# Optimization experiments

Measured on AMD Instinct MI355X. Metric: run time of the kernel, lower is better.

The kernel has to match this reference:

```python
import jax, jax.numpy as jnp
import numpy as np

FP = 2048       # fingerprint / hopf_input_size
A = 1024        # hopf_asso_dim (num_heads = 1)
B = 512         # batch of molecules
T = 50000       # number of templates (memory size)
BETA = 0.125    # hopf_beta


def setup_inputs() -> dict:
    key = jax.random.key(0)
    k_m, k_t, k_wm, k_wt = jax.random.split(key, 4)
    # binary-ish fingerprints approximated with uniform [0,1)
    m = jax.random.uniform(k_m, (B, FP), dtype=jnp.float32)
    templates = jax.random.uniform(k_t, (T, FP), dtype=jnp.float32)
    # kaiming_normal fan_in linear: std = 1/sqrt(fan_in)
    std = 1.0 / np.sqrt(FP)
    W_mol = jax.random.normal(k_wm, (A, FP), dtype=jnp.float32) * std
    b_mol = jnp.zeros((A,), dtype=jnp.float32)
    W_temp = jax.random.normal(k_wt, (A, FP), dtype=jnp.float32) * std
    b_temp = jnp.zeros((A,), dtype=jnp.float32)
    return {"m": m, "templates": templates, "W_mol": W_mol, "b_mol": b_mol,
            "W_temp": W_temp, "b_temp": b_temp}


def reference(m, templates, W_mol, b_mol, W_temp, b_temp):
    # mol encoder: single Linear (last layer -> no activation, dropout=0 eval)
    Xi = m @ W_mol.T + b_mol                 # [B, A] queries
    # template encoder: single Linear -> stored pattern memory
    X = templates @ W_temp.T + b_temp       # [T, A] keys/memory
    # Hopfield association: beta-scaled similarity = logits over templates
    out = BETA * jnp.einsum('ba,ta->bt', Xi, X)   # [B, T]
    return out
```

## Files before the change

kernel.cpp:

```cpp
#include <hip/hip_runtime.h>
#include <cstdint>
#include <cstddef>

typedef __attribute__((ext_vector_type(8))) short short8;
typedef __attribute__((ext_vector_type(8))) _Float16 f16x8;
typedef __attribute__((ext_vector_type(4))) float f32x4;
typedef __attribute__((ext_vector_type(4))) unsigned short u16x4;
typedef unsigned short u16;

#define FP_  2048
#define AD_  1024
#define BB_  512
#define TT_  50000
#define BETA_ 0.125f

__device__ __forceinline__ u16 f2bf(float x){
  uint32_t u = __builtin_bit_cast(uint32_t, x);
  u = (u + 0x7fffu + ((u >> 16) & 1u)) >> 16;
  return (u16)u;
}
__device__ __forceinline__ u16 f2h_bits(float x){
  _Float16 h = (_Float16)x;
  return __builtin_bit_cast(u16, h);
}
__device__ __forceinline__ unsigned int pkrtz_u32(float a, float b){
  return __builtin_bit_cast(unsigned int, __builtin_amdgcn_cvt_pkrtz(a, b));
}

__device__ __forceinline__ void gload_lds16(const void* g, void* l){
  __builtin_amdgcn_global_load_lds((const __attribute__((address_space(1))) void*)g,
                                   (__attribute__((address_space(3))) void*)l,
                                   16, 0, 0);
}

#define SB   __builtin_amdgcn_s_barrier()
#define SCH  __builtin_amdgcn_sched_barrier(0)
#define WAIT_LGKM0 asm volatile("s_waitcnt lgkmcnt(0)" ::: "memory")
#define WAIT_VM(n) asm volatile("s_waitcnt vmcnt(" #n ")" ::: "memory")

__global__ void conv_bf_k(const float* __restrict__ src, u16* __restrict__ dst, int n){
  int i = (blockIdx.x * blockDim.x + threadIdx.x) * 4;
  if (i >= n) return;
  f32x4 v = *reinterpret_cast<const f32x4*>(src + i);
  u16x4 h;
  #pragma unroll
  for (int e = 0; e < 4; ++e) h[e] = f2bf(v[e]);
  *reinterpret_cast<u16x4*>(dst + i) = h;
}

__global__ void conv_bf_T_k(const float* __restrict__ W, u16* __restrict__ outT,
                            int R, int C){
  __shared__ float tile[32][33];
  int c0 = blockIdx.x * 32;
  int r0 = blockIdx.y * 32;
  int tx = threadIdx.x;
  int ty = threadIdx.y;
  #pragma unroll
  for (int i = 0; i < 32; i += 8)
    tile[ty + i][tx] = W[(size_t)(r0 + ty + i) * C + c0 + tx];
  __syncthreads();
  #pragma unroll
  for (int i = 0; i < 32; i += 8){
    float x = tile[tx][ty + i];
    outT[(size_t)(c0 + ty + i) * R + r0 + tx] = f2bf(x);
  }
}

__global__ void dot_rows_k(const float* __restrict__ Xi, const float* __restrict__ bt,
                           float* __restrict__ c, int K){
  int row  = blockIdx.x * 4 + (threadIdx.x >> 6);
  int lane = threadIdx.x & 63;
  float s = 0.f;
  for (int a = lane; a < K; a += 64) s += Xi[(size_t)row * K + a] * bt[a];
  #pragma unroll
  for (int off = 32; off; off >>= 1) s += __shfl_down(s, off);
  if (lane == 0) c[row] = s;
}

template<int TM, int TN, int FM, int FN, int OUT>
__global__ __launch_bounds__(256, 2)
void gemm_s(const u16* __restrict__ A, const u16* __restrict__ B,
            int M, int N, int K,
            float* __restrict__ Cf, u16* __restrict__ C16,
            const float* __restrict__ colBias)
{
  constexpr int BK = 32;
  constexpr int WM = TM / (16 * FM);
  constexpr int WN = TN / (16 * FN);
  static_assert(WM * WN == 4, "4 waves / 256 threads");
  constexpr int BUFE = (TM + TN) * BK;

  __shared__ __align__(16) u16 lds[2 * BUFE];

  const int m0 = blockIdx.x * TM;
  const int n0 = blockIdx.y * TN;

  const int tid  = threadIdx.x;
  const int w    = tid >> 6;
  const int lane = tid & 63;
  const int lr   = lane & 15;
  const int lg   = lane >> 4;
  const int wm   = w / WN;
  const int wn   = w % WN;

  const int rrA = tid >> 2;
  const int chA = tid & 3;

  short8 ra, rb;

  f32x4 acc[FM][FN];
  #pragma unroll
  for (int i = 0; i < FM; ++i)
    #pragma unroll
    for (int j = 0; j < FN; ++j)
      acc[i][j] = (f32x4){0.f, 0.f, 0.f, 0.f};

  auto stage_load = [&](int k0){
    int gm = m0 + rrA;
    ra = *reinterpret_cast<const short8*>(A + (size_t)gm * K + k0 + chA * 8);
    int gn = n0 + rrA; if (gn > N - 1) gn = N - 1;
    rb = *reinterpret_cast<const short8*>(B + (size_t)gn * K + k0 + chA * 8);
  };
  auto stage_store = [&](int buf){
    u16* As = lds + buf * BUFE;
    u16* Bs = As + TM * BK;
    int row = rrA;
    int sw  = (chA ^ ((row >> 1) & 3)) << 3;
    *reinterpret_cast<short8*>(As + row * BK + sw) = ra;
    *reinterpret_cast<short8*>(Bs + row * BK + sw) = rb;
  };

  const int NT = K / BK;
  stage_load(0);
  stage_store(0);
  __syncthreads();

  int cur = 0;
  for (int t = 0; t < NT; ++t){
    const bool have_next = (t + 1 < NT);
    if (have_next) stage_load((t + 1) * BK);

    u16* As = lds + cur * BUFE;
    u16* Bs = As + TM * BK;

    short8 ah[FM], bh[FN];
    #pragma unroll
    for (int i = 0; i < FM; ++i){
      int row = wm * FM * 16 + i * 16 + lr;
      int off = row * BK + ((lg ^ ((row >> 1) & 3)) << 3);
      ah[i] = *reinterpret_cast<short8*>(As + off);
    }
    #pragma unroll
    for (int j = 0; j < FN; ++j){
      int row = wn * FN * 16 + j * 16 + lr;
      int off = row * BK + ((lg ^ ((row >> 1) & 3)) << 3);
      bh[j] = *reinterpret_cast<short8*>(Bs + off);
    }
    #pragma unroll
    for (int i = 0; i < FM; ++i)
      #pragma unroll
      for (int j = 0; j < FN; ++j)
        acc[i][j] = __builtin_amdgcn_mfma_f32_16x16x32_bf16(ah[i], bh[j], acc[i][j], 0, 0, 0);

    if (have_next){
      __builtin_amdgcn_sched_barrier(0);
      stage_store(cur ^ 1);
      __syncthreads();
    }
    cur ^= 1;
  }

  #pragma unroll
  for (int i = 0; i < FM; ++i){
    int rbase = m0 + wm * FM * 16 + i * 16 + lg * 4;
    #pragma unroll
    for (int j = 0; j < FN; ++j){
      int gcol = n0 + wn * FN * 16 + j * 16 + lr;
      if (gcol < N){
        float cb = colBias ? colBias[gcol] : 0.f;
        #pragma unroll
        for (int r = 0; r < 4; ++r){
          int grow = rbase + r;
          float v = acc[i][j][r] + cb;
          size_t idx = (size_t)grow * N + gcol;
          if constexpr (OUT == 1){
            Cf[idx]  = v;
            C16[idx] = f2bf(v);
          } else {
            C16[idx] = f2h_bits(v);
          }
        }
      }
    }
  }
}

__global__ __launch_bounds__(512, 1)
void gemm_big(const u16* __restrict__ Ah,
              const float* __restrict__ Bf,
              float* __restrict__ C,
              const float* __restrict__ rowAdd, float alpha)
{
  constexpr int K = FP_, NN = TT_;
  constexpr int NT = K / 64;
  constexpr int KS = 8192;
  constexpr int BOFF = 16384;
  constexpr int SLOT = 32768;

  __shared__ __align__(16) u16 lds[2 * SLOT];

  int id  = blockIdx.x;
  int xcd = id & 7;
  int g   = id >> 3;
  int mt  = g & 1;
  int sg  = g >> 1;
  int strips = (xcd < 4) ? 25 : 24;
  if (sg >= strips) return;
  int nt = ((xcd < 4) ? xcd * 25 : 100 + (xcd - 4) * 24) + sg;
  const int m0 = mt * 256;
  const int n0 = nt * 256;

  const int tid  = threadIdx.x;
  const int w    = tid >> 6;
  const int lane = tid & 63;
  const int lr   = lane & 15;
  const int lg   = lane >> 4;
  const int wm   = w >> 2;
  const int wn   = w & 3;

  auto glA = [&](u16* sp_, int Tt, int h){
    int rl = lane >> 2;
    int cc = lane & 3;
    int row = h * 128 + w * 16 + rl;
    #pragma unroll
    for (int ks = 0; ks < 2; ++ks){
      const u16* src = Ah + (size_t)(m0 + row) * K + Tt * 64 + ks * 32
                     + ((cc ^ ((row >> 1) & 3)) << 3);
      gload_lds16(src, sp_ + ks * KS + (size_t)(h * 128 + w * 16) * 32);
    }
  };
  auto issueB = [&](int Tt, int h, f32x4 (&rb)[4]){
    #pragma unroll
    for (int p = 0; p < 4; ++p){
      int rl = h * 128 + p * 32 + (tid >> 4);
      int gn = n0 + rl; if (gn > NN - 1) gn = NN - 1;
      rb[p] = *reinterpret_cast<const f32x4*>(Bf + (size_t)gn * K + Tt * 64 + (tid & 15) * 4);
    }
  };
  auto publishB = [&](u16* sp_, int h, f32x4 (&rb)[4]){
    int fch = tid & 15;
    int ks  = fch >> 3;
    int c16 = (fch & 7) >> 1;
    int hf  = fch & 1;
    #pragma unroll
    for (int p = 0; p < 4; ++p){
      int row = h * 128 + p * 32 + (tid >> 4);
      uint2 hv;
      hv.x = pkrtz_u32(rb[p][0], rb[p][1]);
      hv.y = pkrtz_u32(rb[p][2], rb[p][3]);
      int phys = c16 ^ ((row >> 1) & 3);
      *reinterpret_cast<uint2*>(sp_ + BOFF + ks * KS + row * 32 + phys * 8 + hf * 4) = hv;
    }
  };

  f32x4 acc[8][4];
  #pragma unroll
  for (int i = 0; i < 8; ++i)
    #pragma unroll
    for (int j = 0; j < 4; ++j)
      acc[i][j] = (f32x4){0.f, 0.f, 0.f, 0.f};

  f32x4 rbB0[4], rbB1[4];
  f16x8 pa[4][2], pb[2][2];

#define READ_PA(SP, MH)                                                        \
  _Pragma("unroll")                                                            \
  for (int ii = 0; ii < 4; ++ii){                                              \
    int row_ = wm * 128 + ((MH) * 4 + ii) * 16 + lr;                           \
    _Pragma("unroll")                                                          \
    for (int ks_ = 0; ks_ < 2; ++ks_)                                          \
      pa[ii][ks_] = __builtin_bit_cast(f16x8, *reinterpret_cast<short8*>(      \
        (SP) + ks_ * KS + row_ * 32 + ((lg ^ ((row_ >> 1) & 3)) << 3)));       \
  }

#define READ_PB(SP, NH)                                                        \
  _Pragma("unroll")                                                            \
  for (int jj = 0; jj < 2; ++jj){                                              \
    int row_ = wn * 64 + ((NH) * 2 + jj) * 16 + lr;                            \
    _Pragma("unroll")                                                          \
    for (int ks_ = 0; ks_ < 2; ++ks_)                                          \
      pb[jj][ks_] = __builtin_bit_cast(f16x8, *reinterpret_cast<short8*>(      \
        (SP) + BOFF + ks_ * KS + row_ * 32 + ((lg ^ ((row_ >> 1) & 3)) << 3)));\
  }

#define MMA(MH, NH)                                                            \
  __builtin_amdgcn_s_setprio(1);                                               \
  _Pragma("unroll")                                                            \
  for (int ii = 0; ii < 4; ++ii)                                               \
    _Pragma("unroll")                                                          \
    for (int jj = 0; jj < 2; ++jj){                                            \
      acc[(MH)*4+ii][(NH)*2+jj] = __builtin_amdgcn_mfma_f32_16x16x32_f16(      \
          pa[ii][0], pb[jj][0], acc[(MH)*4+ii][(NH)*2+jj], 0, 0, 0);           \
      acc[(MH)*4+ii][(NH)*2+jj] = __builtin_amdgcn_mfma_f32_16x16x32_f16(      \
          pa[ii][1], pb[jj][1], acc[(MH)*4+ii][(NH)*2+jj], 0, 0, 0);           \
    }                                                                          \
  __builtin_amdgcn_s_setprio(0);

  glA(lds, 0, 0);  glA(lds, 0, 1);
  SCH;
  issueB(0, 0, rbB0);
  issueB(0, 1, rbB1);
  SCH;
  WAIT_VM(4); SCH;
  publishB(lds, 0, rbB0);
  WAIT_VM(0); SCH;
  publishB(lds, 1, rbB1);
  SCH;
  issueB(1, 0, rbB0);
  issueB(1, 1, rbB1);
  WAIT_LGKM0;
  SB; SCH;

  for (int T = 0; T < NT; ++T){
    u16* sp  = lds + (size_t)(T & 1) * SLOT;
    u16* spn = lds + (size_t)((T + 1) & 1) * SLOT;
    const bool hasN  = (T + 1 < NT);
    const bool hasNN = (T + 2 < NT);

    READ_PA(sp, 0);
    READ_PB(sp, 0);
    if (hasN) glA(spn, T + 1, 0);
    WAIT_LGKM0; SCH;
    MMA(0, 0);

    READ_PB(sp, 1);
    if (hasN){
      glA(spn, T + 1, 1);
      SCH;
      WAIT_VM(8); SCH;
      publishB(spn, 0, rbB0);
      if (hasNN){ issueB(T + 2, 0, rbB0); SCH; }
    }
    WAIT_LGKM0; SCH;
    MMA(0, 1);

    READ_PA(sp, 1);
    if (hasN){
      if (hasNN) { WAIT_VM(8); } else { WAIT_VM(4); }
      SCH;
      publishB(spn, 1, rbB1);
      if (hasNN){ issueB(T + 2, 1, rbB1); SCH; }
    }
    WAIT_LGKM0; SCH;
    MMA(1, 1);

    READ_PB(sp, 0);
    if (hasN){
      if (hasNN) { WAIT_VM(8); } else { WAIT_VM(0); }
      SCH;
    }
    WAIT_LGKM0; SCH;
    MMA(1, 0);
    SCH;
    SB;
  }

#undef READ_PA
#undef READ_PB
#undef MMA

  #pragma unroll
  for (int i = 0; i < 8; ++i){
    int rbase = m0 + wm * 128 + i * 16 + lg * 4;
    #pragma unroll
    for (int j = 0; j < 4; ++j){
      int gcol = n0 + wn * 64 + j * 16 + lr;
      if (gcol < NN){
        #pragma unroll
        for (int r = 0; r < 4; ++r){
          int grow = rbase + r;
          float v = (acc[i][j][r] + rowAdd[grow]) * alpha;
          C[(size_t)grow * NN + gcol] = v;
        }
      }
    }
  }
}

extern "C" void kernel_launch(void* const* d_in, const int* in_sizes, int n_in,
                              void* d_out, int out_size, void* d_ws, size_t ws_size,
                              hipStream_t stream){
  (void)in_sizes; (void)n_in; (void)out_size; (void)ws_size;
  const float* m    = (const float*)d_in[0];
  const float* tpl  = (const float*)d_in[1];
  const float* Wmol = (const float*)d_in[2];
  const float* bmol = (const float*)d_in[3];
  const float* Wtmp = (const float*)d_in[4];
  const float* btmp = (const float*)d_in[5];
  float* out = (float*)d_out;

  uint8_t* wp = (uint8_t*)d_ws;
  auto carve = [&](size_t bytes) -> void* {
    void* p = (void*)wp;
    wp += (bytes + 255) & ~(size_t)255;
    return p;
  };
  u16* m_bf   = (u16*)carve((size_t)BB_ * FP_ * 2);
  u16* wm_bf  = (u16*)carve((size_t)AD_ * FP_ * 2);
  u16* wtT_bf = (u16*)carve((size_t)FP_ * AD_ * 2);
  float* Xi   = (float*)carve((size_t)BB_ * AD_ * 4);
  u16* Xi_bf  = (u16*)carve((size_t)BB_ * AD_ * 2);
  u16* Y_hi   = (u16*)carve((size_t)BB_ * FP_ * 2);
  float* cvec = (float*)carve((size_t)BB_ * 4);

  conv_bf_k<<<(BB_ * FP_ / 4 + 255) / 256, 256, 0, stream>>>(m, m_bf, BB_ * FP_);
  conv_bf_k<<<(AD_ * FP_ / 4 + 255) / 256, 256, 0, stream>>>(Wmol, wm_bf, AD_ * FP_);
  conv_bf_T_k<<<dim3(FP_ / 32, AD_ / 32), dim3(32, 8), 0, stream>>>(Wtmp, wtT_bf, AD_, FP_);

  gemm_s<64, 64, 2, 2, 1><<<dim3(BB_ / 64, AD_ / 64), 256, 0, stream>>>(
      m_bf, wm_bf, BB_, AD_, FP_, Xi, Xi_bf, bmol);

  dot_rows_k<<<BB_ / 4, 256, 0, stream>>>(Xi, btmp, cvec, AD_);

  gemm_s<64, 64, 2, 2, 2><<<dim3(BB_ / 64, FP_ / 64), 256, 0, stream>>>(
      Xi_bf, wtT_bf, BB_, FP_, AD_, nullptr, Y_hi, nullptr);

  gemm_big<<<400, 512, 0, stream>>>(Y_hi, tpl, out, cvec, BETA_);
}
```

Before: 218.5 us.

## Split big GEMM into full-tile main kernel plus smaller-tile tail kernel

The main GEMM now covers only the first 128 column strips (256 blocks, one 256x256 tile each, evenly spread over XCDs). A new 128x128-tile kernel with 256 threads covers the remaining 68 strips, split into 544 blocks. The goal is to fix wave quantization and load imbalance from 400 large tiles on 256 CUs. The cost is an extra launch and less data reuse per tile in the tail, and the two launches run one after the other on the same stream.

```diff
diff --git a/kernel.cpp b/kernel.cpp
--- a/kernel.cpp
+++ b/kernel.cpp
@@ -214,9 +214,7 @@
   int g   = id >> 3;
   int mt  = g & 1;
   int sg  = g >> 1;
-  int strips = (xcd < 4) ? 25 : 24;
-  if (sg >= strips) return;
-  int nt = ((xcd < 4) ? xcd * 25 : 100 + (xcd - 4) * 24) + sg;
+  int nt  = xcd * 16 + sg;
   const int m0 = mt * 256;
   const int n0 = nt * 256;
 
@@ -387,6 +385,196 @@
   }
 }
 
+__global__ __launch_bounds__(256, 2)
+void gemm_q(const u16* __restrict__ Ah,
+            const float* __restrict__ Bf,
+            float* __restrict__ C,
+            const float* __restrict__ rowAdd, float alpha)
+{
+  constexpr int K = FP_, NN = TT_;
+  constexpr int NT = K / 64;
+  constexpr int KS = 4096;
+  constexpr int BOFF = 8192;
+  constexpr int SLOT = 16384;
+
+  __shared__ __align__(16) u16 lds[2 * SLOT];
+
+  int id   = blockIdx.x;
+  int jobg = (id & 7) * 68 + (id >> 3);
+  int strip = jobg >> 3;
+  int sub   = jobg & 7;
+  int mq    = sub >> 1;
+  int nh    = sub & 1;
+  const int m0 = mq * 128;
+  const int n0 = (128 + strip) * 256 + nh * 128;
+
+  const int tid  = threadIdx.x;
+  const int w    = tid >> 6;
+  const int lane = tid & 63;
+  const int lr   = lane & 15;
+  const int lg   = lane >> 4;
+  const int wm   = w >> 1;
+  const int wn   = w & 1;
+
+  auto glA = [&](u16* sp_, int Tt, int h){
+    int rl = lane >> 2;
+    int cc = lane & 3;
+    int row = h * 64 + w * 16 + rl;
+    #pragma unroll
+    for (int ks = 0; ks < 2; ++ks){
+      const u16* src = Ah + (size_t)(m0 + row) * K + Tt * 64 + ks * 32
+                     + ((cc ^ ((row >> 1) & 3)) << 3);
+      gload_lds16(src, sp_ + ks * KS + (size_t)(h * 64 + w * 16) * 32);
+    }
+  };
+  auto issueB = [&](int Tt, int h, f32x4 (&rb)[4]){
+    #pragma unroll
+    for (int p = 0; p < 4; ++p){
+      int rl = h * 64 + p * 16 + (tid >> 4);
+      int gn = n0 + rl; if (gn > NN - 1) gn = NN - 1;
+      rb[p] = *reinterpret_cast<const f32x4*>(Bf + (size_t)gn * K + Tt * 64 + (tid & 15) * 4);
+    }
+  };
+  auto publishB = [&](u16* sp_, int h, f32x4 (&rb)[4]){
+    int fch = tid & 15;
+    int ks  = fch >> 3;
+    int c16 = (fch & 7) >> 1;
+    int hf  = fch & 1;
+    #pragma unroll
+    for (int p = 0; p < 4; ++p){
+      int row = h * 64 + p * 16 + (tid >> 4);
+      uint2 hv;
+      hv.x = pkrtz_u32(rb[p][0], rb[p][1]);
+      hv.y = pkrtz_u32(rb[p][2], rb[p][3]);
+      int phys = c16 ^ ((row >> 1) & 3);
+      *reinterpret_cast<uint2*>(sp_ + BOFF + ks * KS + row * 32 + phys * 8 + hf * 4) = hv;
+    }
+  };
+
+  f32x4 acc[4][4];
+  #pragma unroll
+  for (int i = 0; i < 4; ++i)
+    #pragma unroll
+    for (int j = 0; j < 4; ++j)
+      acc[i][j] = (f32x4){0.f, 0.f, 0.f, 0.f};
+
+  f32x4 rbB0[4], rbB1[4];
+  f16x8 pa[2][2], pb[2][2];
+
+#define READ_PA(SP, MH)                                                        \
+  _Pragma("unroll")                                                            \
+  for (int ii = 0; ii < 2; ++ii){                                              \
+    int row_ = wm * 64 + ((MH) * 2 + ii) * 16 + lr;                            \
+    _Pragma("unroll")                                                          \
+    for (int ks_ = 0; ks_ < 2; ++ks_)                                          \
+      pa[ii][ks_] = __builtin_bit_cast(f16x8, *reinterpret_cast<short8*>(      \
+        (SP) + ks_ * KS + row_ * 32 + ((lg ^ ((row_ >> 1) & 3)) << 3)));       \
+  }
+
+#define READ_PB(SP, NH)                                                        \
+  _Pragma("unroll")                                                            \
+  for (int jj = 0; jj < 2; ++jj){                                              \
+    int row_ = wn * 64 + ((NH) * 2 + jj) * 16 + lr;                            \
+    _Pragma("unroll")                                                          \
+    for (int ks_ = 0; ks_ < 2; ++ks_)                                          \
+      pb[jj][ks_] = __builtin_bit_cast(f16x8, *reinterpret_cast<short8*>(      \
+        (SP) + BOFF + ks_ * KS + row_ * 32 + ((lg ^ ((row_ >> 1) & 3)) << 3)));\
+  }
+
+#define MMA(MH, NH)                                                            \
+  __builtin_amdgcn_s_setprio(1);                                               \
+  _Pragma("unroll")                                                            \
+  for (int ii = 0; ii < 2; ++ii)                                               \
+    _Pragma("unroll")                                                          \
+    for (int jj = 0; jj < 2; ++jj){                                            \
+      acc[(MH)*2+ii][(NH)*2+jj] = __builtin_amdgcn_mfma_f32_16x16x32_f16(      \
+          pa[ii][0], pb[jj][0], acc[(MH)*2+ii][(NH)*2+jj], 0, 0, 0);           \
+      acc[(MH)*2+ii][(NH)*2+jj] = __builtin_amdgcn_mfma_f32_16x16x32_f16(      \
+          pa[ii][1], pb[jj][1], acc[(MH)*2+ii][(NH)*2+jj], 0, 0, 0);           \
+    }                                                                          \
+  __builtin_amdgcn_s_setprio(0);
+
+  glA(lds, 0, 0);  glA(lds, 0, 1);
+  SCH;
+  issueB(0, 0, rbB0);
+  issueB(0, 1, rbB1);
+  SCH;
+  WAIT_VM(4); SCH;
+  publishB(lds, 0, rbB0);
+  WAIT_VM(0); SCH;
+  publishB(lds, 1, rbB1);
+  SCH;
+  issueB(1, 0, rbB0);
+  issueB(1, 1, rbB1);
+  WAIT_LGKM0;
+  SB; SCH;
+
+  for (int T = 0; T < NT; ++T){
+    u16* sp  = lds + (size_t)(T & 1) * SLOT;
+    u16* spn = lds + (size_t)((T + 1) & 1) * SLOT;
+    const bool hasN  = (T + 1 < NT);
+    const bool hasNN = (T + 2 < NT);
+
+    READ_PA(sp, 0);
+    READ_PB(sp, 0);
+    if (hasN) glA(spn, T + 1, 0);
+    WAIT_LGKM0; SCH;
+    MMA(0, 0);
+
+    READ_PB(sp, 1);
+    if (hasN){
+      glA(spn, T + 1, 1);
+      SCH;
+      WAIT_VM(8); SCH;
+      publishB(spn, 0, rbB0);
+      if (hasNN){ issueB(T + 2, 0, rbB0); SCH; }
+    }
+    WAIT_LGKM0; SCH;
+    MMA(0, 1);
+
+    READ_PA(sp, 1);
+    if (hasN){
+      if (hasNN) { WAIT_VM(8); } else { WAIT_VM(4); }
+      SCH;
+      publishB(spn, 1, rbB1);
+      if (hasNN){ issueB(T + 2, 1, rbB1); SCH; }
+    }
+    WAIT_LGKM0; SCH;
+    MMA(1, 1);
+
+    READ_PB(sp, 0);
+    if (hasN){
+      if (hasNN) { WAIT_VM(8); } else { WAIT_VM(0); }
+      SCH;
+    }
+    WAIT_LGKM0; SCH;
+    MMA(1, 0);
+    SCH;
+    SB;
+  }
+
+#undef READ_PA
+#undef READ_PB
+#undef MMA
+
+  #pragma unroll
+  for (int i = 0; i < 4; ++i){
+    int rbase = m0 + wm * 64 + i * 16 + lg * 4;
+    #pragma unroll
+    for (int j = 0; j < 4; ++j){
+      int gcol = n0 + wn * 64 + j * 16 + lr;
+      if (gcol < NN){
+        #pragma unroll
+        for (int r = 0; r < 4; ++r){
+          int grow = rbase + r;
+          float v = (acc[i][j][r] + rowAdd[grow]) * alpha;
+          C[(size_t)grow * NN + gcol] = v;
+        }
+      }
+    }
+  }
+}
+
 extern "C" void kernel_launch(void* const* d_in, const int* in_sizes, int n_in,
                               void* d_out, int out_size, void* d_ws, size_t ws_size,
                               hipStream_t stream){
@@ -425,5 +613,6 @@
   gemm_s<64, 64, 2, 2, 2><<<dim3(BB_ / 64, FP_ / 64), 256, 0, stream>>>(
       Xi_bf, wtT_bf, BB_, FP_, AD_, nullptr, Y_hi, nullptr);
 
-  gemm_big<<<400, 512, 0, stream>>>(Y_hi, tpl, out, cvec, BETA_);
-}
+  gemm_big<<<256, 512, 0, stream>>>(Y_hi, tpl, out, cvec, BETA_);
+  gemm_q<<<544, 256, 0, stream>>>(Y_hi, tpl, out, cvec, BETA_);
+}
```

Measured after the change: 248.3 us. 13.6% more time.
